# Kernel optimization log

Hardware: AMD Instinct MI355X
Metric: run time of the kernel (lower is better)

## Reference

```python
import jax, jax.numpy as jnp
import numpy as np

D_MODEL = 512
CONTEXT_LENGTH = 128


def setup_inputs() -> dict:
    key = jax.random.key(0)
    k1, k2, k3, k4 = jax.random.split(key, 4)
    B, T, C = 512, 128, D_MODEL
    H = 64  # head_size
    x = jax.random.normal(k1, (B, T, C), dtype=jnp.float32)
    # torch nn.Linear(d_model, head_size, bias=False) stores weight as [head_size, d_model]
    s = 1.0 / np.sqrt(C)
    Wq = jax.random.uniform(k2, (H, C), dtype=jnp.float32, minval=-s, maxval=s)
    Wk = jax.random.uniform(k3, (H, C), dtype=jnp.float32, minval=-s, maxval=s)
    Wv = jax.random.uniform(k4, (H, C), dtype=jnp.float32, minval=-s, maxval=s)
    return {"x": x, "Wq": Wq, "Wk": Wk, "Wv": Wv}


def reference(x, Wq, Wk, Wv):
    # x: [B, T, C]; Wq/Wk/Wv: [H, C] (torch Linear weight layout, y = x @ W^T)
    B, T, C = x.shape
    H = Wq.shape[0]
    Q = jnp.einsum('btc,hc->bth', x, Wq)  # [B, T, H]
    K = jnp.einsum('btc,hc->bth', x, Wk)
    V = jnp.einsum('btc,hc->bth', x, Wv)
    scale = 1.0 / jnp.sqrt(jnp.asarray(H, dtype=x.dtype))
    scores = jnp.einsum('bth,bsh->bts', Q, K) * scale  # [B, T, T]
    causal = jnp.tril(jnp.ones((T, T), dtype=bool))
    scores = jnp.where(causal, scores, jnp.asarray(-jnp.inf, dtype=scores.dtype))
    weights = jax.nn.softmax(scores, axis=-1)
    # dropout is identity in eval mode (reference baseline)
    out = jnp.einsum('bts,bsh->bth', weights, V)  # [B, T, H]
    return out
```

## Files before the change

kernel.cpp:

```cpp
#include <hip/hip_runtime.h>
#include <hip/hip_bf16.h>


#define TT 128
#define CC 512
#define HH 64

typedef __attribute__((ext_vector_type(8))) short bf16x8;
typedef __attribute__((ext_vector_type(4))) float f32x4;

__device__ __forceinline__ ushort f2bf(float f) {
    union { float f; unsigned u; } v; v.f = f;
    unsigned r = v.u + 0x7fffu + ((v.u >> 16) & 1u);
    return (ushort)(r >> 16);
}

__device__ __forceinline__ void gload_lds16(const void* g, void* l) {
    __builtin_amdgcn_global_load_lds(
        (const __attribute__((address_space(1))) unsigned int*)g,
        (__attribute__((address_space(3))) unsigned int*)l, 16, 0, 0);
}

__global__ void wpack_kernel(const float* __restrict__ wq,
                             const float* __restrict__ wk,
                             const float* __restrict__ wv,
                             ushort* __restrict__ wpk) {
    int p = blockIdx.x * 256 + threadIdx.x;
    int j  = p & 7;
    int l  = (p >> 3) & 63;
    int nt = (p >> 9) % 12;
    int kt = p / (12 * 512);
    int w  = nt >> 2;
    const float* src = (w == 0) ? wq : ((w == 1) ? wk : wv);
    int h = (nt & 3) * 16 + (l & 15);
    int c = kt * 32 + ((l >> 4) << 3) + j;
    wpk[kt * 8192 + ((nt * 64 + l) * 8) + j] = f2bf(src[h * 512 + c]);
}

__launch_bounds__(512, 4)
__global__ void attn_fused_kernel(const float* __restrict__ x,
                                  const ushort* __restrict__ wpk,
                                  float* __restrict__ out) {
    __shared__ __align__(16) char smem[49152];
    ushort* qs  = (ushort*)smem;
    ushort* ks  = (ushort*)(smem + 16384);
    ushort* vst = (ushort*)(smem + 32768);
    ushort* ps  = (ushort*)smem;

    const int tid  = threadIdx.x;
    const int wave = tid >> 6;
    const int lane = tid & 63;
    const int lq   = lane >> 4;
    const int lr   = lane & 15;
    const int b    = blockIdx.x;
    const size_t bB = (size_t)b * TT;

    const f32x4 fzero = {0.f, 0.f, 0.f, 0.f};

    f32x4 acc[12];
    #pragma unroll
    for (int j = 0; j < 12; ++j) acc[j] = fzero;

    const int r = wave * 16 + lr;
    const float* xr = x + (bB + r) * CC + lq * 8;

    auto stageW = [&](int kt, int s) {
        const char* wsrc = (const char*)wpk + kt * 16384;
        char* wdst = smem + s * 16384;
        #pragma unroll
        for (int p = 0; p < 2; ++p) {
            int off = wave * 2048 + p * 1024;
            gload_lds16(wsrc + off + lane * 16, wdst + off);
        }
    };

    #define LOADX(kt, dlo, dhi)                                                \
        {                                                                      \
            const float* p0 = xr + (kt) * 32;                                  \
            asm volatile("global_load_dwordx4 %0, %1, off"                     \
                         : "=&v"(dlo) : "v"(p0) : "memory");                   \
            asm volatile("global_load_dwordx4 %0, %1, off offset:16"           \
                         : "=&v"(dhi) : "v"(p0) : "memory");                   \
        }

    f32x4 x0a, x0b, x1a, x1b, x2a, x2b;

    stageW(0, 0);
    stageW(1, 1);
    LOADX(0, x0a, x0b);
    LOADX(1, x1a, x1b);

    #pragma unroll
    for (int kt = 0; kt < 16; ++kt) {
        const int cur = kt % 3;

        __builtin_amdgcn_s_barrier();

        if (kt + 2 < 16) {
            stageW(kt + 2, (kt + 2) % 3);
            const int slot = (kt + 2) % 3;
            if (slot == 0)      LOADX(kt + 2, x0a, x0b)
            else if (slot == 1) LOADX(kt + 2, x1a, x1b)
            else                LOADX(kt + 2, x2a, x2b)
        }

        if (kt == 0)       asm volatile("s_waitcnt vmcnt(6)" ::: "memory");
        else if (kt <= 13) asm volatile("s_waitcnt vmcnt(8)" ::: "memory");
        else if (kt == 14) asm volatile("s_waitcnt vmcnt(4)" ::: "memory");
        else               asm volatile("s_waitcnt vmcnt(0)" ::: "memory");
        __builtin_amdgcn_sched_barrier(0);

        __builtin_amdgcn_s_barrier();
        __builtin_amdgcn_sched_barrier(0);

        f32x4 alo, ahi;
        if (cur == 0)      { alo = x0a; ahi = x0b; }
        else if (cur == 1) { alo = x1a; ahi = x1b; }
        else               { alo = x2a; ahi = x2b; }
        bf16x8 a;
        a[0] = (short)f2bf(alo[0]); a[1] = (short)f2bf(alo[1]);
        a[2] = (short)f2bf(alo[2]); a[3] = (short)f2bf(alo[3]);
        a[4] = (short)f2bf(ahi[0]); a[5] = (short)f2bf(ahi[1]);
        a[6] = (short)f2bf(ahi[2]); a[7] = (short)f2bf(ahi[3]);

        const ushort* wf = (const ushort*)(smem + cur * 16384);
        #pragma unroll
        for (int g = 0; g < 3; ++g) {
            bf16x8 w0 = *(const bf16x8*)(wf + ((g * 4 + 0) * 64 + lane) * 8);
            bf16x8 w1 = *(const bf16x8*)(wf + ((g * 4 + 1) * 64 + lane) * 8);
            bf16x8 w2 = *(const bf16x8*)(wf + ((g * 4 + 2) * 64 + lane) * 8);
            bf16x8 w3 = *(const bf16x8*)(wf + ((g * 4 + 3) * 64 + lane) * 8);
            acc[g * 4 + 0] = __builtin_amdgcn_mfma_f32_16x16x32_bf16(a, w0, acc[g * 4 + 0], 0, 0, 0);
            acc[g * 4 + 1] = __builtin_amdgcn_mfma_f32_16x16x32_bf16(a, w1, acc[g * 4 + 1], 0, 0, 0);
            acc[g * 4 + 2] = __builtin_amdgcn_mfma_f32_16x16x32_bf16(a, w2, acc[g * 4 + 2], 0, 0, 0);
            acc[g * 4 + 3] = __builtin_amdgcn_mfma_f32_16x16x32_bf16(a, w3, acc[g * 4 + 3], 0, 0, 0);
        }
    }

    __syncthreads();

    #pragma unroll
    for (int nt = 0; nt < 12; ++nt)
        #pragma unroll
        for (int j = 0; j < 4; ++j) {
            int t = wave * 16 + lq * 4 + j;
            int h = (nt & 3) * 16 + lr;
            ushort v = f2bf(acc[nt][j]);
            if (nt < 4)      qs[t * 64 + (h ^ ((t & 7) << 3))] = v;
            else if (nt < 8) ks[t * 64 + (h ^ ((t & 7) << 3))] = v;
            else             vst[h * 128 + (t ^ ((h & 7) << 3))] = v;
        }
    __syncthreads();

    const int row0 = wave * 16;
    f32x4 s[8];
    #pragma unroll
    for (int j = 0; j < 8; ++j) s[j] = fzero;

    #pragma unroll
    for (int kt = 0; kt < 2; ++kt) {
        int h0 = kt * 32 + lq * 8;
        int t  = row0 + lr;
        bf16x8 a = *(const bf16x8*)&qs[t * 64 + (h0 ^ ((t & 7) << 3))];
        bf16x8 kf[8];
        #pragma unroll
        for (int nt = 0; nt < 8; ++nt) {
            int sc = nt * 16 + lr;
            kf[nt] = *(const bf16x8*)&ks[sc * 64 + (h0 ^ ((sc & 7) << 3))];
        }
        #pragma unroll
        for (int nt = 0; nt < 8; ++nt)
            s[nt] = __builtin_amdgcn_mfma_f32_16x16x32_bf16(a, kf[nt], s[nt], 0, 0, 0);
    }

    float rinv[4];
    #pragma unroll
    for (int j = 0; j < 4; ++j) {
        int t = row0 + lq * 4 + j;
        float m = -1e30f;
        #pragma unroll
        for (int nt = 0; nt < 8; ++nt) {
            int sc = nt * 16 + lr;
            float v = s[nt][j] * 0.125f;
            v = (sc <= t) ? v : -1e30f;
            s[nt][j] = v;
            m = fmaxf(m, v);
        }
        m = fmaxf(m, __shfl_xor(m, 1));
        m = fmaxf(m, __shfl_xor(m, 2));
        m = fmaxf(m, __shfl_xor(m, 4));
        m = fmaxf(m, __shfl_xor(m, 8));
        float sum = 0.f;
        #pragma unroll
        for (int nt = 0; nt < 8; ++nt) {
            float p = __expf(s[nt][j] - m);
            s[nt][j] = p;
            sum += p;
        }
        sum += __shfl_xor(sum, 1);
        sum += __shfl_xor(sum, 2);
        sum += __shfl_xor(sum, 4);
        sum += __shfl_xor(sum, 8);
        rinv[j] = 1.0f / sum;
    }

    __syncthreads();

    #pragma unroll
    for (int j = 0; j < 4; ++j) {
        int t = row0 + lq * 4 + j;
        #pragma unroll
        for (int nt = 0; nt < 8; ++nt) {
            int sc = nt * 16 + lr;
            ps[t * 128 + (sc ^ ((t & 7) << 3))] = f2bf(s[nt][j]);
        }
    }
    __syncthreads();

    f32x4 o[4];
    #pragma unroll
    for (int j = 0; j < 4; ++j) o[j] = fzero;

    #pragma unroll
    for (int ksv = 0; ksv < 4; ++ksv) {
        int s0 = ksv * 32 + lq * 8;
        int t  = row0 + lr;
        bf16x8 a = *(const bf16x8*)&ps[t * 128 + (s0 ^ ((t & 7) << 3))];
        bf16x8 vf[4];
        #pragma unroll
        for (int nt = 0; nt < 4; ++nt) {
            int h = nt * 16 + lr;
            vf[nt] = *(const bf16x8*)&vst[h * 128 + (s0 ^ ((h & 7) << 3))];
        }
        #pragma unroll
        for (int nt = 0; nt < 4; ++nt)
            o[nt] = __builtin_amdgcn_mfma_f32_16x16x32_bf16(a, vf[nt], o[nt], 0, 0, 0);
    }

    float* ob = out + (size_t)b * (TT * HH);
    #pragma unroll
    for (int nt = 0; nt < 4; ++nt)
        #pragma unroll
        for (int j = 0; j < 4; ++j) {
            int t = row0 + lq * 4 + j;
            int h = nt * 16 + lr;
            ob[t * HH + h] = o[nt][j] * rinv[j];
        }
}

extern "C" void kernel_launch(void* const* d_in, const int* in_sizes, int n_in,
                              void* d_out, int out_size, void* d_ws, size_t ws_size,
                              hipStream_t stream) {
    const float* x  = (const float*)d_in[0];
    const float* wq = (const float*)d_in[1];
    const float* wk = (const float*)d_in[2];
    const float* wv = (const float*)d_in[3];
    float* o = (float*)d_out;
    ushort* wpk = (ushort*)d_ws;

    (void)in_sizes; (void)n_in; (void)out_size; (void)ws_size;

    wpack_kernel<<<384, 256, 0, stream>>>(wq, wk, wv, wpk);
    attn_fused_kernel<<<512, 512, 0, stream>>>(x, wpk, o);
}
```

Measured before the change: 39.39 us.

## Separate P from QKV in LDS, drop syncs, double-buffer W staging

Shared memory grows so that the P tile no longer aliases the Q/K/V buffers. This lets two block-wide barriers around the probability write be removed, since each wave only reads its own rows. The projection loop now double-buffers W tiles with a prefetch distance of one instead of a triple buffer, and it issues all 12 W fragment reads before the MFMAs. V-transposed stores are vectorized to 4-element writes. The larger LDS footprint lowers the number of blocks that can reside per CU, and the shorter W prefetch distance may expose more load latency.

```diff
diff --git a/kernel.cpp b/kernel.cpp
--- a/kernel.cpp
+++ b/kernel.cpp
@@ -7,6 +7,7 @@
 #define HH 64
 
 typedef __attribute__((ext_vector_type(8))) short bf16x8;
+typedef __attribute__((ext_vector_type(4))) ushort u16x4;
 typedef __attribute__((ext_vector_type(4))) float f32x4;
 
 __device__ __forceinline__ ushort f2bf(float f) {
@@ -41,11 +42,11 @@
 __global__ void attn_fused_kernel(const float* __restrict__ x,
                                   const ushort* __restrict__ wpk,
                                   float* __restrict__ out) {
-    __shared__ __align__(16) char smem[49152];
-    ushort* qs  = (ushort*)smem;
-    ushort* ks  = (ushort*)(smem + 16384);
-    ushort* vst = (ushort*)(smem + 32768);
+    __shared__ __align__(16) char smem[81920];
     ushort* ps  = (ushort*)smem;
+    ushort* qs  = (ushort*)(smem + 32768);
+    ushort* ks  = (ushort*)(smem + 49152);
+    ushort* vst = (ushort*)(smem + 65536);
 
     const int tid  = threadIdx.x;
     const int wave = tid >> 6;
@@ -86,7 +87,6 @@
     f32x4 x0a, x0b, x1a, x1b, x2a, x2b;
 
     stageW(0, 0);
-    stageW(1, 1);
     LOADX(0, x0a, x0b);
     LOADX(1, x1a, x1b);
 
@@ -96,16 +96,15 @@
 
         __builtin_amdgcn_s_barrier();
 
+        if (kt + 1 < 16) stageW(kt + 1, (kt + 1) & 1);
         if (kt + 2 < 16) {
-            stageW(kt + 2, (kt + 2) % 3);
             const int slot = (kt + 2) % 3;
             if (slot == 0)      LOADX(kt + 2, x0a, x0b)
             else if (slot == 1) LOADX(kt + 2, x1a, x1b)
             else                LOADX(kt + 2, x2a, x2b)
         }
 
-        if (kt == 0)       asm volatile("s_waitcnt vmcnt(6)" ::: "memory");
-        else if (kt <= 13) asm volatile("s_waitcnt vmcnt(8)" ::: "memory");
+        if (kt <= 13)      asm volatile("s_waitcnt vmcnt(6)" ::: "memory");
         else if (kt == 14) asm volatile("s_waitcnt vmcnt(4)" ::: "memory");
         else               asm volatile("s_waitcnt vmcnt(0)" ::: "memory");
         __builtin_amdgcn_sched_barrier(0);
@@ -123,33 +122,39 @@
         a[4] = (short)f2bf(ahi[0]); a[5] = (short)f2bf(ahi[1]);
         a[6] = (short)f2bf(ahi[2]); a[7] = (short)f2bf(ahi[3]);
 
-        const ushort* wf = (const ushort*)(smem + cur * 16384);
-        #pragma unroll
-        for (int g = 0; g < 3; ++g) {
-            bf16x8 w0 = *(const bf16x8*)(wf + ((g * 4 + 0) * 64 + lane) * 8);
-            bf16x8 w1 = *(const bf16x8*)(wf + ((g * 4 + 1) * 64 + lane) * 8);
-            bf16x8 w2 = *(const bf16x8*)(wf + ((g * 4 + 2) * 64 + lane) * 8);
-            bf16x8 w3 = *(const bf16x8*)(wf + ((g * 4 + 3) * 64 + lane) * 8);
-            acc[g * 4 + 0] = __builtin_amdgcn_mfma_f32_16x16x32_bf16(a, w0, acc[g * 4 + 0], 0, 0, 0);
-            acc[g * 4 + 1] = __builtin_amdgcn_mfma_f32_16x16x32_bf16(a, w1, acc[g * 4 + 1], 0, 0, 0);
-            acc[g * 4 + 2] = __builtin_amdgcn_mfma_f32_16x16x32_bf16(a, w2, acc[g * 4 + 2], 0, 0, 0);
-            acc[g * 4 + 3] = __builtin_amdgcn_mfma_f32_16x16x32_bf16(a, w3, acc[g * 4 + 3], 0, 0, 0);
-        }
-    }
-
-    __syncthreads();
-
-    #pragma unroll
-    for (int nt = 0; nt < 12; ++nt)
-        #pragma unroll
-        for (int j = 0; j < 4; ++j) {
-            int t = wave * 16 + lq * 4 + j;
+        const ushort* wf = (const ushort*)(smem + (kt & 1) * 16384);
+        bf16x8 w[12];
+        #pragma unroll
+        for (int nt = 0; nt < 12; ++nt)
+            w[nt] = *(const bf16x8*)(wf + (nt * 64 + lane) * 8);
+        #pragma unroll
+        for (int nt = 0; nt < 12; ++nt)
+            acc[nt] = __builtin_amdgcn_mfma_f32_16x16x32_bf16(a, w[nt], acc[nt], 0, 0, 0);
+    }
+
+    {
+        const int t0 = wave * 16 + lq * 4;
+        #pragma unroll
+        for (int nt = 0; nt < 8; ++nt) {
+            #pragma unroll
+            for (int j = 0; j < 4; ++j) {
+                int t = t0 + j;
+                int h = (nt & 3) * 16 + lr;
+                ushort v = f2bf(acc[nt][j]);
+                if (nt < 4) qs[t * 64 + (h ^ ((t & 7) << 3))] = v;
+                else        ks[t * 64 + (h ^ ((t & 7) << 3))] = v;
+            }
+        }
+        #pragma unroll
+        for (int nt = 8; nt < 12; ++nt) {
             int h = (nt & 3) * 16 + lr;
-            ushort v = f2bf(acc[nt][j]);
-            if (nt < 4)      qs[t * 64 + (h ^ ((t & 7) << 3))] = v;
-            else if (nt < 8) ks[t * 64 + (h ^ ((t & 7) << 3))] = v;
-            else             vst[h * 128 + (t ^ ((h & 7) << 3))] = v;
-        }
+            int base = t0 ^ ((h & 7) << 3);
+            u16x4 v4;
+            v4[0] = f2bf(acc[nt][0]); v4[1] = f2bf(acc[nt][1]);
+            v4[2] = f2bf(acc[nt][2]); v4[3] = f2bf(acc[nt][3]);
+            *(u16x4*)&vst[h * 128 + base] = v4;
+        }
+    }
     __syncthreads();
 
     const int row0 = wave * 16;
@@ -204,8 +209,6 @@
         rinv[j] = 1.0f / sum;
     }
 
-    __syncthreads();
-
     #pragma unroll
     for (int j = 0; j < 4; ++j) {
         int t = row0 + lq * 4 + j;
@@ -215,7 +218,6 @@
             ps[t * 128 + (sc ^ ((t & 7) << 3))] = f2bf(s[nt][j]);
         }
     }
-    __syncthreads();
 
     f32x4 o[4];
     #pragma unroll
```

After: 39.27 us. Within noise of the previous version (-0.3%).
